# Performance work log

Hardware: AMD Instinct MI355X
Metric: run time of the kernel (lower is better)

The kernel has to match this reference:

```python
import jax, jax.numpy as jnp
import numpy as np

N_NODES = 50000
DEG = 16                      # uniform in-degree so every node receives messages (matches dgl mailbox semantics)
N_EDGES = N_NODES * DEG       # 800000
IND = 128
EDIM = 64
OUT = 128
AVG_D = float(np.log(DEG + 1.0))   # PNA avg_d['log']
EPS = 1e-5


def setup_inputs() -> dict:
    key = jax.random.key(0)
    k = jax.random.split(key, 6)
    h = jax.random.normal(k[0], (N_NODES, IND), dtype=jnp.float32)
    ef = jax.random.normal(k[1], (N_EDGES, EDIM), dtype=jnp.float32)
    src = jax.random.randint(k[2], (N_EDGES,), 0, N_NODES)
    dst = jnp.repeat(jnp.arange(N_NODES), DEG)  # every node has exactly DEG incoming edges
    pre_in = 2 * IND + EDIM            # 320
    post_in = IND * (1 + 4 * 3)        # 1664: h + 4 aggregators x 3 scalers
    W_pre = jax.random.normal(k[3], (pre_in, IND), dtype=jnp.float32) * (1.0 / np.sqrt(pre_in))
    b_pre = jnp.zeros((IND,), dtype=jnp.float32)
    W_post = jax.random.normal(k[4], (post_in, OUT), dtype=jnp.float32) * (1.0 / np.sqrt(post_in))
    b_post = jnp.zeros((OUT,), dtype=jnp.float32)
    return {"h": h, "ef": ef, "src": src, "dst": dst,
            "W_pre": W_pre, "b_pre": b_pre, "W_post": W_post, "b_post": b_post}


def reference(h, ef, src, dst, W_pre, b_pre, W_post, b_post):
    n = h.shape[0]
    # --- pretrans on edges: cat(src_h, dst_h, ef) -> Linear ---
    z2 = jnp.concatenate([h[src], h[dst], ef], axis=1)          # [E, 2*IND+EDIM]
    e = z2 @ W_pre + b_pre                                       # [E, IND]
    # --- multi-aggregator segment reduce over incoming edges (by dst) ---
    deg = jax.ops.segment_sum(jnp.ones((e.shape[0],), e.dtype), dst, num_segments=n)  # [N]
    safe_deg = jnp.maximum(deg, 1.0)[:, None]
    s1 = jax.ops.segment_sum(e, dst, num_segments=n)
    s2 = jax.ops.segment_sum(e * e, dst, num_segments=n)
    mean = s1 / safe_deg
    std = jnp.sqrt(jax.nn.relu(s2 / safe_deg - mean * mean) + EPS)
    mx = jax.ops.segment_max(e, dst, num_segments=n)
    mn = jax.ops.segment_min(e, dst, num_segments=n)
    has = (deg > 0)[:, None]
    mx = jnp.where(has, mx, 0.0)
    mn = jnp.where(has, mn, 0.0)
    agg = jnp.concatenate([mean, mx, mn, std], axis=1)           # [N, 4*IND]
    # --- scalers: identity, amplification log(D+1)/avg_d, attenuation avg_d/log(D+1) ---
    logd = jnp.log(deg + 1.0)
    amp = (logd / AVG_D)[:, None]
    att = (AVG_D / jnp.maximum(logd, 1e-6))[:, None]
    att = jnp.where(deg[:, None] > 0, att, 0.0)
    scaled = jnp.concatenate([agg, agg * amp, agg * att], axis=1)  # [N, 12*IND]
    # --- posttrans on nodes: cat(h, aggregated) -> Linear ---
    hcat = jnp.concatenate([h, scaled], axis=1)                  # [N, 13*IND]
    return hcat @ W_post + b_post                                # [N, OUT]
```

## Files before the change

kernel.cpp:

```cpp
#include <hip/hip_runtime.h>

#define N_NODES 50000
#define IND 128
#define EDIM 64

typedef __bf16 bf16x8 __attribute__((ext_vector_type(8)));
typedef float  f32x4  __attribute__((ext_vector_type(4)));
typedef unsigned short u16x8 __attribute__((ext_vector_type(8)));

__device__ __forceinline__ unsigned short f2bfu(float f) {
  __bf16 b = (__bf16)f;
  return __builtin_bit_cast(unsigned short, b);
}
__device__ __forceinline__ float bfu2f(unsigned short u) {
  __bf16 b = __builtin_bit_cast(__bf16, u);
  return (float)b;
}
__device__ __forceinline__ f32x4 mfma16(bf16x8 a, bf16x8 b, f32x4 c) {
  return __builtin_amdgcn_mfma_f32_16x16x32_bf16(a, b, c, 0, 0, 0);
}
__device__ __forceinline__ bf16x8 pack8(float4 a, float4 b) {
  bf16x8 r;
  r[0]=(__bf16)a.x; r[1]=(__bf16)a.y; r[2]=(__bf16)a.z; r[3]=(__bf16)a.w;
  r[4]=(__bf16)b.x; r[5]=(__bf16)b.y; r[6]=(__bf16)b.z; r[7]=(__bf16)b.w;
  return r;
}

__global__ __launch_bounds__(256) void pack_weights(const float* W_pre, const float* W_post,
                                                    unsigned short* WpreF, unsigned short* WcF,
                                                    unsigned short* WfoldF) {
  int idx = blockIdx.x * 256 + threadIdx.x;
  if (idx < 32768) {
    int j = idx & 7, lane = (idx >> 3) & 63, ct = (idx >> 9) & 15, kb = idx >> 13;
    int k = kb * 32 + (lane >> 4) * 8 + j;
    int col = ct * 16 + (lane & 15);
    float v = (col < 128) ? W_pre[k * 128 + col] : W_pre[(128 + k) * 128 + (col - 128)];
    WpreF[idx] = f2bfu(v);
  } else if (idx < 32768 + 8192) {
    int i = idx - 32768;
    int j = i & 7, lane = (i >> 3) & 63, ct = (i >> 9) & 7, kb = i >> 12;
    int k = kb * 32 + (lane >> 4) * 8 + j;
    int col = ct * 16 + (lane & 15);
    WcF[i] = f2bfu(W_pre[(256 + k) * 128 + col]);
  } else if (idx < 122880) {
    int i = idx - 40960;
    int j = i & 7, lane = (i >> 3) & 63, ct = (i >> 9) & 7, kb = i >> 12;
    int k = kb * 32 + (lane >> 4) * 8 + j;
    int col = ct * 16 + (lane & 15);
    float v;
    if (k < 128) {
      v = W_post[k * 128 + col];
    } else {
      int p = k - 128;
      int t = p >> 7;
      int c = ((p & 7) * 16) + ((p >> 3) & 15);
      size_t r0 = 128 + (size_t)t * 128 + c;
      v = W_post[r0 * 128 + col] + W_post[(r0 + 512) * 128 + col] +
          W_post[(r0 + 1024) * 128 + col];
    }
    WfoldF[i] = f2bfu(v);
  }
}

__global__ __launch_bounds__(256) void pre_gemm(const float* h, const unsigned short* WpreF,
                                                const float* b_pre,
                                                unsigned short* haB, float* hbP) {
  int lane = threadIdx.x & 63;
  int gw = blockIdx.x * 4 + (threadIdx.x >> 6);
  size_t base = (size_t)gw * 16;
  if (base >= N_NODES) return;
  int q = lane >> 4, c16 = lane & 15;
  f32x4 acc[16];
#pragma unroll
  for (int i = 0; i < 16; i++) acc[i] = (f32x4){0.f, 0.f, 0.f, 0.f};
#pragma unroll
  for (int kb = 0; kb < 4; kb++) {
    const float* hp = h + (base + c16) * 128 + kb * 32 + q * 8;
    float4 lo = *(const float4*)hp;
    float4 hi = *(const float4*)(hp + 4);
    bf16x8 a = pack8(lo, hi);
#pragma unroll
    for (int ct = 0; ct < 16; ct++) {
      bf16x8 b = *(const bf16x8*)(WpreF + ((size_t)(kb * 16 + ct) * 64 + lane) * 8);
      acc[ct] = mfma16(a, b, acc[ct]);
    }
  }
  float bp[8];
#pragma unroll
  for (int ct = 0; ct < 8; ct++) bp[ct] = b_pre[ct * 16 + c16];
#pragma unroll
  for (int r = 0; r < 4; r++) {
    size_t row = base + q * 4 + r;
    u16x8 hv;
#pragma unroll
    for (int ct = 0; ct < 8; ct++) hv[ct] = f2bfu(acc[ct][r]);
    *(u16x8*)(haB + row * 128 + c16 * 8) = hv;
    float4 w0 = {acc[8][r] + bp[0], acc[9][r] + bp[1], acc[10][r] + bp[2], acc[11][r] + bp[3]};
    float4 w1 = {acc[12][r] + bp[4], acc[13][r] + bp[5], acc[14][r] + bp[6], acc[15][r] + bp[7]};
    *(float4*)(hbP + row * 128 + c16 * 8) = w0;
    *(float4*)(hbP + row * 128 + c16 * 8 + 4) = w1;
  }
}

__global__ __launch_bounds__(256, 6) void edge_agg(const float* ef, const int* src,
                                                   const unsigned short* haB, const float* hbP,
                                                   const unsigned short* WcF,
                                                   unsigned short* aggB) {
  __shared__ unsigned short ldsWc[8192];
  {
    const int4* g = (const int4*)WcF;
    int4* l = (int4*)ldsWc;
#pragma unroll
    for (int i = 0; i < 4; i++) l[threadIdx.x + i * 256] = g[threadIdx.x + i * 256];
  }
  int lane = threadIdx.x & 63, wib = threadIdx.x >> 6;
  int q = lane >> 4, c16 = lane & 15;
  int n = blockIdx.x * 4 + wib;
  int srcv = src[n * 16 + c16];
  const float* ep0 = ef + ((size_t)n * 16 + c16) * 64 + q * 8;
  float4 Ea = *(const float4*)ep0;
  float4 Eb = *(const float4*)(ep0 + 4);
  float4 Ec = *(const float4*)(ep0 + 32);
  float4 Ed = *(const float4*)(ep0 + 36);
  const float* hbp = hbP + (size_t)n * 128 + c16 * 8;
  float4 H0 = *(const float4*)hbp;
  float4 H1 = *(const float4*)(hbp + 4);
  u16x8 G[4];
#pragma unroll
  for (int r = 0; r < 4; r++) {
    int s = __shfl(srcv, q * 4 + r, 64);
    G[r] = *(const u16x8*)(haB + (size_t)s * 128 + c16 * 8);
  }
  __syncthreads();
  bf16x8 a0 = pack8(Ea, Eb), a1 = pack8(Ec, Ed);
  f32x4 acc[8];
#pragma unroll
  for (int ct = 0; ct < 8; ct++) {
    bf16x8 b = *(const bf16x8*)(ldsWc + ((size_t)ct * 64 + lane) * 8);
    acc[ct] = mfma16(a0, b, (f32x4){0.f, 0.f, 0.f, 0.f});
  }
#pragma unroll
  for (int ct = 0; ct < 8; ct++) {
    bf16x8 b = *(const bf16x8*)(ldsWc + ((size_t)(8 + ct) * 64 + lane) * 8);
    acc[ct] = mfma16(a1, b, acc[ct]);
  }
  float hb[8] = {H0.x, H0.y, H0.z, H0.w, H1.x, H1.y, H1.z, H1.w};
  u16x8 ov;
#pragma unroll
  for (int ct = 0; ct < 8; ct++) {
    float sum = 0.f, s2 = 0.f, mx = -3.4e38f, mn = 3.4e38f;
#pragma unroll
    for (int r = 0; r < 4; r++) {
      float e = acc[ct][r] + bfu2f(G[r][ct]);
      sum += e; s2 = __builtin_fmaf(e, e, s2);
      mx = fmaxf(mx, e); mn = fminf(mn, e);
    }
    sum += __shfl_xor(sum, 16, 64); s2 += __shfl_xor(s2, 16, 64);
    mx = fmaxf(mx, __shfl_xor(mx, 16, 64)); mn = fminf(mn, __shfl_xor(mn, 16, 64));
    sum += __shfl_xor(sum, 32, 64); s2 += __shfl_xor(s2, 32, 64);
    mx = fmaxf(mx, __shfl_xor(mx, 32, 64)); mn = fminf(mn, __shfl_xor(mn, 32, 64));
    float mean = sum * 0.0625f;
    float var = fmaxf(s2 * 0.0625f - mean * mean, 0.f);
    float sd = sqrtf(var + 1e-5f);
    float v = (q == 0) ? mean : (q == 1) ? mx : (q == 2) ? mn : sd;
    if (q != 3) v += hb[ct];
    ov[ct] = f2bfu(v);
  }
  *(u16x8*)(aggB + (size_t)n * 512 + lane * 8) = ov;
}

__global__ __launch_bounds__(256) void post_gemm(const float* h, const unsigned short* aggB,
                                                 const unsigned short* WfoldF,
                                                 const float* b_post, float* out) {
  int lane = threadIdx.x & 63;
  int gw = blockIdx.x * 4 + (threadIdx.x >> 6);
  size_t base = (size_t)gw * 16;
  if (base >= N_NODES) return;
  int q = lane >> 4, c16 = lane & 15;
  size_t r0 = base + c16;
  f32x4 acc[8];
#pragma unroll
  for (int i = 0; i < 8; i++) acc[i] = (f32x4){0.f, 0.f, 0.f, 0.f};
  float4 fa, fb; u16x8 ua;
  {
    const float* p = h + r0 * 128 + q * 8;
    fa = *(const float4*)p; fb = *(const float4*)(p + 4);
  }
  for (int kb = 0; kb < 20; kb++) {
    bf16x8 a = (kb < 4) ? pack8(fa, fb) : __builtin_bit_cast(bf16x8, ua);
    if (kb + 1 < 4) {
      const float* p = h + r0 * 128 + (kb + 1) * 32 + q * 8;
      fa = *(const float4*)p; fb = *(const float4*)(p + 4);
    } else if (kb + 1 < 20) {
      ua = *(const u16x8*)(aggB + r0 * 512 + (size_t)(kb + 1 - 4) * 32 + q * 8);
    }
#pragma unroll
    for (int ct = 0; ct < 8; ct++) {
      bf16x8 b = *(const bf16x8*)(WfoldF + ((size_t)(kb * 8 + ct) * 64 + lane) * 8);
      acc[ct] = mfma16(a, b, acc[ct]);
    }
  }
#pragma unroll
  for (int ct = 0; ct < 8; ct++) {
    int col = ct * 16 + c16;
    float bp = b_post[col];
#pragma unroll
    for (int r = 0; r < 4; r++) {
      size_t row = base + q * 4 + r;
      out[row * 128 + col] = acc[ct][r] + bp;
    }
  }
}

extern "C" void kernel_launch(void* const* d_in, const int* in_sizes, int n_in,
                              void* d_out, int out_size, void* d_ws, size_t ws_size,
                              hipStream_t stream) {
  const float* h      = (const float*)d_in[0];
  const float* ef     = (const float*)d_in[1];
  const int*   src    = (const int*)d_in[2];
  const float* W_pre  = (const float*)d_in[4];
  const float* b_pre  = (const float*)d_in[5];
  const float* W_post = (const float*)d_in[6];
  const float* b_post = (const float*)d_in[7];
  float* out = (float*)d_out;

  char* ws = (char*)d_ws;
  unsigned short* haB    = (unsigned short*)ws;
  float*          hbP    = (float*)(haB + (size_t)N_NODES * 128);
  unsigned short* aggB   = (unsigned short*)(hbP + (size_t)N_NODES * 128);
  unsigned short* WpreF  = aggB + (size_t)N_NODES * 512;
  unsigned short* WcF    = WpreF + 32768;
  unsigned short* WfoldF = WcF + 8192;
  (void)in_sizes; (void)n_in; (void)out_size; (void)ws_size;

  pack_weights<<<480, 256, 0, stream>>>(W_pre, W_post, WpreF, WcF, WfoldF);
  pre_gemm<<<782, 256, 0, stream>>>(h, WpreF, b_pre, haB, hbP);
  edge_agg<<<12500, 256, 0, stream>>>(ef, src, haB, hbP, WcF, aggB);
  post_gemm<<<782, 256, 0, stream>>>(h, aggB, WfoldF, b_post, out);
}
```

Baseline: 425.7 us.

## Fold destination-node pretrans term and bias algebraically into post-GEMM weights

Each edge's h[dst]·W_pre_b + b_pre term is constant within a node's mailbox, so it shifts mean, max and min by the same per-node vector and leaves std unchanged. The change drops the hbP buffer and its per-edge read, and instead folds W_pre_b times the summed scaler weights into the h-block of the folded post weights. The b_pre contribution goes into a new bias vector. It also makes post_gemm process 32 rows per wave, so each weight fragment load feeds two MFMAs. The gain is less memory traffic (no fp32 hbP write or read) and less pre-GEMM work, in exchange for a more complex weight-packing kernel. The folded weights are rounded to bf16 after an extra product, which may shift precision.

```diff
diff --git a/kernel.cpp b/kernel.cpp
--- a/kernel.cpp
+++ b/kernel.cpp
@@ -26,53 +26,87 @@
   return r;
 }
 
-__global__ __launch_bounds__(256) void pack_weights(const float* W_pre, const float* W_post,
-                                                    unsigned short* WpreF, unsigned short* WcF,
-                                                    unsigned short* WfoldF) {
-  int idx = blockIdx.x * 256 + threadIdx.x;
-  if (idx < 32768) {
-    int j = idx & 7, lane = (idx >> 3) & 63, ct = (idx >> 9) & 15, kb = idx >> 13;
-    int k = kb * 32 + (lane >> 4) * 8 + j;
-    int col = ct * 16 + (lane & 15);
-    float v = (col < 128) ? W_pre[k * 128 + col] : W_pre[(128 + k) * 128 + (col - 128)];
-    WpreF[idx] = f2bfu(v);
-  } else if (idx < 32768 + 8192) {
-    int i = idx - 32768;
-    int j = i & 7, lane = (i >> 3) & 63, ct = (i >> 9) & 7, kb = i >> 12;
-    int k = kb * 32 + (lane >> 4) * 8 + j;
-    int col = ct * 16 + (lane & 15);
-    WcF[i] = f2bfu(W_pre[(256 + k) * 128 + col]);
-  } else if (idx < 122880) {
-    int i = idx - 40960;
-    int j = i & 7, lane = (i >> 3) & 63, ct = (i >> 9) & 7, kb = i >> 12;
-    int k = kb * 32 + (lane >> 4) * 8 + j;
-    int col = ct * 16 + (lane & 15);
-    float v;
-    if (k < 128) {
-      v = W_post[k * 128 + col];
-    } else {
-      int p = k - 128;
-      int t = p >> 7;
-      int c = ((p & 7) * 16) + ((p >> 3) & 15);
-      size_t r0 = 128 + (size_t)t * 128 + c;
-      v = W_post[r0 * 128 + col] + W_post[(r0 + 512) * 128 + col] +
-          W_post[(r0 + 1024) * 128 + col];
-    }
-    WfoldF[i] = f2bfu(v);
+__global__ __launch_bounds__(256) void pack_all(const float* W_pre, const float* W_post,
+                                                const float* b_pre, const float* b_post,
+                                                unsigned short* WpreF, unsigned short* WcF,
+                                                unsigned short* WfoldF, float* bias2) {
+  __shared__ float ldsW[16384];
+  int b = blockIdx.x, t = threadIdx.x;
+  if (b < 16) {
+    for (int i = 0; i < 64; i++) {
+      int idx = t + i * 256;
+      int c = idx >> 7, col = idx & 127;
+      float s = 0.f;
+#pragma unroll
+      for (int sc = 0; sc < 3; sc++)
+#pragma unroll
+        for (int st = 0; st < 3; st++)
+          s += W_post[(size_t)(128 + sc * 512 + st * 128 + c) * 128 + col];
+      ldsW[idx] = s;
+    }
+    __syncthreads();
+    int col = t & 127, kh = t >> 7;
+    for (int i = 0; i < 4; i++) {
+      int k = b * 8 + i * 2 + kh;
+      float a0 = W_post[(size_t)k * 128 + col], a1 = 0.f, a2 = 0.f, a3 = 0.f;
+      const float* wb = W_pre + (size_t)(128 + k) * 128;
+#pragma unroll 4
+      for (int c = 0; c < 128; c += 4) {
+        a0 = fmaf(wb[c],     ldsW[c * 128 + col], a0);
+        a1 = fmaf(wb[c + 1], ldsW[(c + 1) * 128 + col], a1);
+        a2 = fmaf(wb[c + 2], ldsW[(c + 2) * 128 + col], a2);
+        a3 = fmaf(wb[c + 3], ldsW[(c + 3) * 128 + col], a3);
+      }
+      float acc = (a0 + a1) + (a2 + a3);
+      int kb = k >> 5, j = k & 7, qq = (k >> 3) & 3;
+      int lane = qq * 16 + (col & 15), ct = col >> 4;
+      WfoldF[((size_t)(kb * 8 + ct) * 64 + lane) * 8 + j] = f2bfu(acc);
+    }
+    if (b == 0 && t < 128) {
+      int col = t;
+      float acc = b_post[col];
+      for (int c = 0; c < 128; c++) acc = fmaf(b_pre[c], ldsW[c * 128 + col], acc);
+      bias2[col] = acc;
+    }
+  } else {
+    int idx = (b - 16) * 256 + t;
+    if (idx < 16384) {
+      int j = idx & 7, lane = (idx >> 3) & 63, ct = (idx >> 9) & 7, kb = idx >> 12;
+      int k = kb * 32 + (lane >> 4) * 8 + j;
+      int col = ct * 16 + (lane & 15);
+      WpreF[idx] = f2bfu(W_pre[k * 128 + col]);
+    } else if (idx < 24576) {
+      int i = idx - 16384;
+      int j = i & 7, lane = (i >> 3) & 63, ct = (i >> 9) & 7, kb = i >> 12;
+      int k = kb * 32 + (lane >> 4) * 8 + j;
+      int col = ct * 16 + (lane & 15);
+      WcF[i] = f2bfu(W_pre[(256 + k) * 128 + col]);
+    } else if (idx < 24576 + 65536) {
+      int i = idx - 24576;
+      int j = i & 7, lane = (i >> 3) & 63, ct = (i >> 9) & 7, kbr = i >> 12;
+      int kb = kbr + 4;
+      int p = kbr * 32 + ((lane >> 4) & 3) * 8 + j;
+      int tt = p >> 7;
+      int c = (p & 7) * 16 + ((p >> 3) & 15);
+      int col = ct * 16 + (lane & 15);
+      size_t r0 = 128 + (size_t)tt * 128 + c;
+      float v = W_post[r0 * 128 + col] + W_post[(r0 + 512) * 128 + col] +
+                W_post[(r0 + 1024) * 128 + col];
+      WfoldF[((size_t)(kb * 8 + ct) * 64 + lane) * 8 + j] = f2bfu(v);
+    }
   }
 }
 
 __global__ __launch_bounds__(256) void pre_gemm(const float* h, const unsigned short* WpreF,
-                                                const float* b_pre,
-                                                unsigned short* haB, float* hbP) {
+                                                unsigned short* haB) {
   int lane = threadIdx.x & 63;
   int gw = blockIdx.x * 4 + (threadIdx.x >> 6);
   size_t base = (size_t)gw * 16;
   if (base >= N_NODES) return;
   int q = lane >> 4, c16 = lane & 15;
-  f32x4 acc[16];
-#pragma unroll
-  for (int i = 0; i < 16; i++) acc[i] = (f32x4){0.f, 0.f, 0.f, 0.f};
+  f32x4 acc[8];
+#pragma unroll
+  for (int i = 0; i < 8; i++) acc[i] = (f32x4){0.f, 0.f, 0.f, 0.f};
 #pragma unroll
   for (int kb = 0; kb < 4; kb++) {
     const float* hp = h + (base + c16) * 128 + kb * 32 + q * 8;
@@ -80,14 +114,11 @@
     float4 hi = *(const float4*)(hp + 4);
     bf16x8 a = pack8(lo, hi);
 #pragma unroll
-    for (int ct = 0; ct < 16; ct++) {
-      bf16x8 b = *(const bf16x8*)(WpreF + ((size_t)(kb * 16 + ct) * 64 + lane) * 8);
+    for (int ct = 0; ct < 8; ct++) {
+      bf16x8 b = *(const bf16x8*)(WpreF + ((size_t)(kb * 8 + ct) * 64 + lane) * 8);
       acc[ct] = mfma16(a, b, acc[ct]);
     }
   }
-  float bp[8];
-#pragma unroll
-  for (int ct = 0; ct < 8; ct++) bp[ct] = b_pre[ct * 16 + c16];
 #pragma unroll
   for (int r = 0; r < 4; r++) {
     size_t row = base + q * 4 + r;
@@ -95,15 +126,11 @@
 #pragma unroll
     for (int ct = 0; ct < 8; ct++) hv[ct] = f2bfu(acc[ct][r]);
     *(u16x8*)(haB + row * 128 + c16 * 8) = hv;
-    float4 w0 = {acc[8][r] + bp[0], acc[9][r] + bp[1], acc[10][r] + bp[2], acc[11][r] + bp[3]};
-    float4 w1 = {acc[12][r] + bp[4], acc[13][r] + bp[5], acc[14][r] + bp[6], acc[15][r] + bp[7]};
-    *(float4*)(hbP + row * 128 + c16 * 8) = w0;
-    *(float4*)(hbP + row * 128 + c16 * 8 + 4) = w1;
   }
 }
 
 __global__ __launch_bounds__(256, 6) void edge_agg(const float* ef, const int* src,
-                                                   const unsigned short* haB, const float* hbP,
+                                                   const unsigned short* haB,
                                                    const unsigned short* WcF,
                                                    unsigned short* aggB) {
   __shared__ unsigned short ldsWc[8192];
@@ -122,9 +149,6 @@
   float4 Eb = *(const float4*)(ep0 + 4);
   float4 Ec = *(const float4*)(ep0 + 32);
   float4 Ed = *(const float4*)(ep0 + 36);
-  const float* hbp = hbP + (size_t)n * 128 + c16 * 8;
-  float4 H0 = *(const float4*)hbp;
-  float4 H1 = *(const float4*)(hbp + 4);
   u16x8 G[4];
 #pragma unroll
   for (int r = 0; r < 4; r++) {
@@ -144,7 +168,6 @@
     bf16x8 b = *(const bf16x8*)(ldsWc + ((size_t)(8 + ct) * 64 + lane) * 8);
     acc[ct] = mfma16(a1, b, acc[ct]);
   }
-  float hb[8] = {H0.x, H0.y, H0.z, H0.w, H1.x, H1.y, H1.z, H1.w};
   u16x8 ov;
 #pragma unroll
   for (int ct = 0; ct < 8; ct++) {
@@ -163,7 +186,6 @@
     float var = fmaxf(s2 * 0.0625f - mean * mean, 0.f);
     float sd = sqrtf(var + 1e-5f);
     float v = (q == 0) ? mean : (q == 1) ? mx : (q == 2) ? mn : sd;
-    if (q != 3) v += hb[ct];
     ov[ct] = f2bfu(v);
   }
   *(u16x8*)(aggB + (size_t)n * 512 + lane * 8) = ov;
@@ -171,45 +193,58 @@
 
 __global__ __launch_bounds__(256) void post_gemm(const float* h, const unsigned short* aggB,
                                                  const unsigned short* WfoldF,
-                                                 const float* b_post, float* out) {
+                                                 const float* bias2, float* out) {
   int lane = threadIdx.x & 63;
   int gw = blockIdx.x * 4 + (threadIdx.x >> 6);
-  size_t base = (size_t)gw * 16;
+  size_t base = (size_t)gw * 32;
   if (base >= N_NODES) return;
   int q = lane >> 4, c16 = lane & 15;
   size_t r0 = base + c16;
-  f32x4 acc[8];
-#pragma unroll
-  for (int i = 0; i < 8; i++) acc[i] = (f32x4){0.f, 0.f, 0.f, 0.f};
-  float4 fa, fb; u16x8 ua;
+  size_t r1 = base + 16 + c16;
+  if (r1 > N_NODES - 1) r1 = N_NODES - 1;
+  f32x4 acc[2][8];
+#pragma unroll
+  for (int i = 0; i < 2; i++)
+#pragma unroll
+    for (int j = 0; j < 8; j++) acc[i][j] = (f32x4){0.f, 0.f, 0.f, 0.f};
+  float4 fa0, fb0, fa1, fb1; u16x8 ua0, ua1;
   {
-    const float* p = h + r0 * 128 + q * 8;
-    fa = *(const float4*)p; fb = *(const float4*)(p + 4);
+    const float* p0 = h + r0 * 128 + q * 8;
+    fa0 = *(const float4*)p0; fb0 = *(const float4*)(p0 + 4);
+    const float* p1 = h + r1 * 128 + q * 8;
+    fa1 = *(const float4*)p1; fb1 = *(const float4*)(p1 + 4);
   }
   for (int kb = 0; kb < 20; kb++) {
-    bf16x8 a = (kb < 4) ? pack8(fa, fb) : __builtin_bit_cast(bf16x8, ua);
+    bf16x8 a0 = (kb < 4) ? pack8(fa0, fb0) : __builtin_bit_cast(bf16x8, ua0);
+    bf16x8 a1 = (kb < 4) ? pack8(fa1, fb1) : __builtin_bit_cast(bf16x8, ua1);
     if (kb + 1 < 4) {
-      const float* p = h + r0 * 128 + (kb + 1) * 32 + q * 8;
-      fa = *(const float4*)p; fb = *(const float4*)(p + 4);
+      const float* p0 = h + r0 * 128 + (kb + 1) * 32 + q * 8;
+      fa0 = *(const float4*)p0; fb0 = *(const float4*)(p0 + 4);
+      const float* p1 = h + r1 * 128 + (kb + 1) * 32 + q * 8;
+      fa1 = *(const float4*)p1; fb1 = *(const float4*)(p1 + 4);
     } else if (kb + 1 < 20) {
-      ua = *(const u16x8*)(aggB + r0 * 512 + (size_t)(kb + 1 - 4) * 32 + q * 8);
+      ua0 = *(const u16x8*)(aggB + r0 * 512 + (size_t)(kb + 1 - 4) * 32 + q * 8);
+      ua1 = *(const u16x8*)(aggB + r1 * 512 + (size_t)(kb + 1 - 4) * 32 + q * 8);
     }
 #pragma unroll
     for (int ct = 0; ct < 8; ct++) {
       bf16x8 b = *(const bf16x8*)(WfoldF + ((size_t)(kb * 8 + ct) * 64 + lane) * 8);
-      acc[ct] = mfma16(a, b, acc[ct]);
-    }
-  }
-#pragma unroll
-  for (int ct = 0; ct < 8; ct++) {
-    int col = ct * 16 + c16;
-    float bp = b_post[col];
-#pragma unroll
-    for (int r = 0; r < 4; r++) {
-      size_t row = base + q * 4 + r;
-      out[row * 128 + col] = acc[ct][r] + bp;
-    }
-  }
+      acc[0][ct] = mfma16(a0, b, acc[0][ct]);
+      acc[1][ct] = mfma16(a1, b, acc[1][ct]);
+    }
+  }
+#pragma unroll
+  for (int rt = 0; rt < 2; rt++)
+#pragma unroll
+    for (int ct = 0; ct < 8; ct++) {
+      int col = ct * 16 + c16;
+      float bp = bias2[col];
+#pragma unroll
+      for (int r = 0; r < 4; r++) {
+        size_t row = base + rt * 16 + q * 4 + r;
+        if (row < N_NODES) out[row * 128 + col] = acc[rt][ct][r] + bp;
+      }
+    }
 }
 
 extern "C" void kernel_launch(void* const* d_in, const int* in_sizes, int n_in,
@@ -226,15 +261,15 @@
 
   char* ws = (char*)d_ws;
   unsigned short* haB    = (unsigned short*)ws;
-  float*          hbP    = (float*)(haB + (size_t)N_NODES * 128);
-  unsigned short* aggB   = (unsigned short*)(hbP + (size_t)N_NODES * 128);
+  unsigned short* aggB   = haB + (size_t)N_NODES * 128;
   unsigned short* WpreF  = aggB + (size_t)N_NODES * 512;
-  unsigned short* WcF    = WpreF + 32768;
+  unsigned short* WcF    = WpreF + 16384;
   unsigned short* WfoldF = WcF + 8192;
+  float*          bias2  = (float*)(WfoldF + 81920);
   (void)in_sizes; (void)n_in; (void)out_size; (void)ws_size;
 
-  pack_weights<<<480, 256, 0, stream>>>(W_pre, W_post, WpreF, WcF, WfoldF);
-  pre_gemm<<<782, 256, 0, stream>>>(h, WpreF, b_pre, haB, hbP);
-  edge_agg<<<12500, 256, 0, stream>>>(ef, src, haB, hbP, WcF, aggB);
-  post_gemm<<<782, 256, 0, stream>>>(h, aggB, WfoldF, b_post, out);
-}
+  pack_all<<<368, 256, 0, stream>>>(W_pre, W_post, b_pre, b_post, WpreF, WcF, WfoldF, bias2);
+  pre_gemm<<<782, 256, 0, stream>>>(h, WpreF, haB);
+  edge_agg<<<12500, 256, 0, stream>>>(ef, src, haB, WcF, aggB);
+  post_gemm<<<391, 256, 0, stream>>>(h, aggB, WfoldF, bias2, out);
+}
```

Result: faster. 403.4 us (-5.3%).
